# Optimization experiments

Hardware: AMD Instinct MI355X
Metric: run time of the kernel (lower is better)

## Reference

```python
import jax, jax.numpy as jnp
import numpy as np
import math

NUM_HEADS = 16


def setup_inputs() -> dict:
    key = jax.random.key(0)
    ks = jax.random.split(key, 7)
    B, S, D = 2, 2048, 1024
    scale = 1.0 / math.sqrt(D)
    return {
        "query": jax.random.normal(ks[0], (B, S, D), jnp.float32),
        "key": jax.random.normal(ks[1], (B, S, D), jnp.float32),
        "value": jax.random.normal(ks[2], (B, S, D), jnp.float32),
        "Wq": jax.random.normal(ks[3], (D, D), jnp.float32) * scale,
        "Wk": jax.random.normal(ks[4], (D, D), jnp.float32) * scale,
        "Wv": jax.random.normal(ks[5], (D, D), jnp.float32) * scale,
        "Wo": jax.random.normal(ks[6], (D, D), jnp.float32) * scale,
    }


def reference(query, key, value, Wq, Wk, Wv, Wo):
    B, Sq, D = query.shape
    Sk = key.shape[1]
    H = NUM_HEADS
    dk = D // H
    # torch Linear (no bias): y = x @ W.T
    q = (query @ Wq.T).reshape(B, Sq, H, dk).transpose(0, 2, 1, 3)  # [B,H,Sq,dk]
    k = (key @ Wk.T).reshape(B, Sk, H, dk).transpose(0, 2, 1, 3)
    v = (value @ Wv.T).reshape(B, Sk, H, dk).transpose(0, 2, 1, 3)
    scores = jnp.einsum("bhqd,bhkd->bhqk", q, k) / jnp.sqrt(jnp.float32(dk))
    causal = jnp.tril(jnp.ones((Sq, Sk), dtype=bool))  # mask_future=True
    scores = jnp.where(causal[None, None], scores, jnp.float32(-1e9))
    p = jax.nn.softmax(scores, axis=-1)
    x = jnp.einsum("bhqk,bhkd->bhqd", p, v)  # [B,H,Sq,dk]
    x = x.transpose(0, 2, 1, 3).reshape(B, Sq, D)
    return x @ Wo.T
```

## Files before the change

kernel.cpp:

```cpp
#include <hip/hip_runtime.h>
#include <hip/hip_bf16.h>
#include <stdint.h>

#define D_MODEL 1024
#define NHEADS  16
#define DK      64
#define SEQ     2048
#define BATCH   2

typedef __bf16 bf16x8 __attribute__((ext_vector_type(8)));
typedef __bf16 bf16x4 __attribute__((ext_vector_type(4)));
typedef float  f32x4  __attribute__((ext_vector_type(4)));

__device__ __forceinline__ void async_copy16(const void* g, void* l) {
  __builtin_amdgcn_global_load_lds(
      (__attribute__((address_space(1))) void*)g,
      (__attribute__((address_space(3))) void*)l, 16, 0, 0);
}

__global__ void cast_all(const float* __restrict__ q, const float* __restrict__ k,
                         const float* __restrict__ v, const float* __restrict__ wq,
                         const float* __restrict__ wk, const float* __restrict__ wv,
                         const float* __restrict__ wo,
                         __bf16* __restrict__ oq, __bf16* __restrict__ ok,
                         __bf16* __restrict__ ov, __bf16* __restrict__ owq,
                         __bf16* __restrict__ owk, __bf16* __restrict__ owv,
                         __bf16* __restrict__ owo) {
  constexpr unsigned Q4 = (unsigned)(BATCH * SEQ * D_MODEL) / 4;
  constexpr unsigned W4 = (unsigned)(D_MODEL * D_MODEL) / 4;
  unsigned i = blockIdx.x * 256u + threadIdx.x;
  const float* in; __bf16* out; unsigned off;
  if (i < 3 * Q4) {
    unsigned z = i >> 20; off = i & (Q4 - 1);
    in  = z == 0 ? q : z == 1 ? k : v;
    out = z == 0 ? oq : z == 1 ? ok : ov;
  } else {
    unsigned j = i - 3 * Q4;
    unsigned z = j >> 18; off = j & (W4 - 1);
    in  = z == 0 ? wq : z == 1 ? wk : z == 2 ? wv : wo;
    out = z == 0 ? owq : z == 1 ? owk : z == 2 ? owv : owo;
  }
  float4 val = *(const float4*)(in + (size_t)off * 4);
  bf16x4 o;
  o.x = (__bf16)val.x; o.y = (__bf16)val.y; o.z = (__bf16)val.z; o.w = (__bf16)val.w;
  *(bf16x4*)(out + (size_t)off * 4) = o;
}

__global__ __launch_bounds__(256, 3)
void gemm_proj(const __bf16* __restrict__ A0, const __bf16* __restrict__ A1, const __bf16* __restrict__ A2,
               const __bf16* __restrict__ B0, const __bf16* __restrict__ B1, const __bf16* __restrict__ B2,
               __bf16* __restrict__ Qp, __bf16* __restrict__ Kp, __bf16* __restrict__ Vt) {
  constexpr int K = D_MODEL, N = D_MODEL;
  const int zi = blockIdx.z;
  const __bf16* A; const __bf16* Bm;
  if (zi == 0)      { A = A0; Bm = B0; }
  else if (zi == 1) { A = A1; Bm = B1; }
  else              { A = A2; Bm = B2; }

  __shared__ __align__(16) char smem[34816];
  __bf16* Ash = (__bf16*)smem;
  __bf16* Bsh = (__bf16*)(smem + 16384);
  __bf16* Tr  = (__bf16*)smem;

  const int tid  = threadIdx.x;
  const int lane = tid & 63;
  const int w    = tid >> 6;
  const int quad = lane >> 4;
  const int l16  = lane & 15;
  const int wr   = w >> 1, wc = w & 1;
  const size_t m0 = (size_t)blockIdx.x * 128;
  const size_t n0 = (size_t)blockIdx.y * 128;

  f32x4 acc[4][4] = {};

  for (int k0 = 0; k0 < K; k0 += 64) {
#pragma unroll
    for (int it = 0; it < 4; ++it) {
      int slot = tid + it * 256;
      int row = slot >> 3, ch = slot & 7;
      async_copy16(A + (m0 + row) * K + k0 + ((ch ^ (row & 7)) * 8), &Ash[slot * 8]);
    }
#pragma unroll
    for (int it = 0; it < 4; ++it) {
      int slot = tid + it * 256;
      int row = slot >> 3, ch = slot & 7;
      async_copy16(Bm + (n0 + row) * K + k0 + ((ch ^ (row & 7)) * 8), &Bsh[slot * 8]);
    }
    __syncthreads();
#pragma unroll
    for (int kk = 0; kk < 2; ++kk) {
      bf16x8 af[4], bfr[4];
#pragma unroll
      for (int i = 0; i < 4; ++i) {
        int row = wr * 64 + i * 16 + l16;
        af[i] = *(const bf16x8*)&Ash[row * 64 + (((kk * 4 + quad) ^ (row & 7)) * 8)];
      }
#pragma unroll
      for (int j = 0; j < 4; ++j) {
        int row = wc * 64 + j * 16 + l16;
        bfr[j] = *(const bf16x8*)&Bsh[row * 64 + (((kk * 4 + quad) ^ (row & 7)) * 8)];
      }
#pragma unroll
      for (int i = 0; i < 4; ++i)
#pragma unroll
        for (int j = 0; j < 4; ++j)
          acc[i][j] = __builtin_amdgcn_mfma_f32_16x16x32_bf16(af[i], bfr[j], acc[i][j], 0, 0, 0);
    }
    __syncthreads();
  }

  if (zi != 2) {
    __bf16* C = (zi == 0) ? Qp : Kp;
#pragma unroll
    for (int i = 0; i < 4; ++i)
#pragma unroll
      for (int j = 0; j < 4; ++j)
#pragma unroll
        for (int r = 0; r < 4; ++r) {
          size_t row = m0 + wr * 64 + i * 16 + quad * 4 + r;
          size_t col = n0 + wc * 64 + j * 16 + l16;
          C[row * N + col] = (__bf16)acc[i][j][r];
        }
  } else {
#pragma unroll
    for (int i = 0; i < 4; ++i)
#pragma unroll
      for (int j = 0; j < 4; ++j)
#pragma unroll
        for (int r = 0; r < 4; ++r)
          Tr[(wc * 64 + j * 16 + l16) * 136 + (wr * 64 + i * 16 + quad * 4 + r)] =
              (__bf16)acc[i][j][r];
    __syncthreads();
    const int b_  = (int)(m0 >> 11);
    const int sl0 = (int)(m0 & 2047);
#pragma unroll
    for (int it = 0; it < 8; ++it) {
      int slot = tid + it * 256;
      int d = slot >> 4, sc = slot & 15;
      *(int4*)&Vt[((size_t)(b_ * D_MODEL) + n0 + d) * SEQ + sl0 + sc * 8] =
          *(const int4*)&Tr[d * 136 + sc * 8];
    }
  }
}

__global__ __launch_bounds__(256, 2)
void gemm_out(const __bf16* __restrict__ A, const __bf16* __restrict__ Bm,
              float* __restrict__ C) {
  constexpr int BM = 64, BN = 128, K = D_MODEL, N = D_MODEL;
  __shared__ __bf16 Ash[BM * 64];
  __shared__ __bf16 Bsh[BN * 64];

  const int tid  = threadIdx.x;
  const int lane = tid & 63;
  const int w    = tid >> 6;
  const int quad = lane >> 4;
  const int l16  = lane & 15;
  const int wr   = w >> 1, wc = w & 1;
  const size_t m0 = (size_t)blockIdx.x * BM;
  const size_t n0 = (size_t)blockIdx.y * BN;

  f32x4 acc[2][4] = {};

  for (int k0 = 0; k0 < K; k0 += 64) {
#pragma unroll
    for (int it = 0; it < 2; ++it) {
      int slot = tid + it * 256;
      int row = slot >> 3, ch = slot & 7;
      async_copy16(A + (m0 + row) * K + k0 + ((ch ^ (row & 7)) * 8), &Ash[slot * 8]);
    }
#pragma unroll
    for (int it = 0; it < 4; ++it) {
      int slot = tid + it * 256;
      int row = slot >> 3, ch = slot & 7;
      async_copy16(Bm + (n0 + row) * K + k0 + ((ch ^ (row & 7)) * 8), &Bsh[slot * 8]);
    }
    __syncthreads();
#pragma unroll
    for (int kk = 0; kk < 2; ++kk) {
      bf16x8 af[2], bfr[4];
#pragma unroll
      for (int i = 0; i < 2; ++i) {
        int row = wr * 32 + i * 16 + l16;
        af[i] = *(const bf16x8*)&Ash[row * 64 + (((kk * 4 + quad) ^ (row & 7)) * 8)];
      }
#pragma unroll
      for (int j = 0; j < 4; ++j) {
        int row = wc * 64 + j * 16 + l16;
        bfr[j] = *(const bf16x8*)&Bsh[row * 64 + (((kk * 4 + quad) ^ (row & 7)) * 8)];
      }
#pragma unroll
      for (int i = 0; i < 2; ++i)
#pragma unroll
        for (int j = 0; j < 4; ++j)
          acc[i][j] = __builtin_amdgcn_mfma_f32_16x16x32_bf16(af[i], bfr[j], acc[i][j], 0, 0, 0);
    }
    __syncthreads();
  }

#pragma unroll
  for (int i = 0; i < 2; ++i)
#pragma unroll
    for (int j = 0; j < 4; ++j)
#pragma unroll
      for (int r = 0; r < 4; ++r) {
        size_t row = m0 + wr * 32 + i * 16 + quad * 4 + r;
        size_t col = n0 + wc * 64 + j * 16 + l16;
        C[row * N + col] = acc[i][j][r];
      }
}

#define PS_W 40

__global__ __launch_bounds__(256, 3)
void attn_kernel(const __bf16* __restrict__ Qp, const __bf16* __restrict__ Kp,
                 const __bf16* __restrict__ Vt, __bf16* __restrict__ Xo) {
  __shared__ __bf16 Kb[2 * 2 * 64 * 32];
  __shared__ __bf16 Vb[2 * 2 * 64 * 32];
  __shared__ __bf16 Ps[4 * 32 * PS_W];
  __shared__ float  Xch[2 * 16 * 66];
  __shared__ float  Lsum[2 * 32];

  const int tid  = threadIdx.x;
  const int lane = tid & 63;
  const int w    = tid >> 6;
  const int qh   = w >> 1, kh = w & 1;
  const int quad = lane >> 4;
  const int l16  = lane & 15;
  const int bh   = blockIdx.x;
  const int qt   = 31 - blockIdx.y;
  const int b    = bh >> 4, h = bh & 15;
  const int q0   = qt * 64;
  const size_t baseRow = (size_t)b * SEQ;
  const int colBase = h * DK;

  const int srow = w * 16 + (lane >> 2);
  const int sk   = (lane & 3) * 8;
  const int skz  = (((lane & 3) ^ ((lane >> 3) & 3)) * 8);
  const int swz  = (l16 >> 1) & 3;

  const float c1 = 0.18033688011f;
  const float c2 = -23.083120654f;

  bf16x8 aq[2][2];
  {
    const __bf16* qrow = Qp + (baseRow + q0 + qh * 32 + l16) * D_MODEL + colBase;
#pragma unroll
    for (int mt = 0; mt < 2; ++mt)
#pragma unroll
      for (int kd = 0; kd < 2; ++kd)
        aq[mt][kd] = *(const bf16x8*)(qrow + (size_t)mt * 16 * D_MODEL + kd * 32 + quad * 8);
  }

  f32x4 oacc[2][4] = {};
  float plsum[2][4] = {};

  {
    const __bf16* kbase = Kp + (baseRow + srow) * D_MODEL + colBase + skz;
    async_copy16(kbase,      &Kb[0 * 2048 + srow * 32 + sk]);
    async_copy16(kbase + 32, &Kb[1 * 2048 + srow * 32 + sk]);
    const __bf16* vbase = Vt + ((size_t)b * D_MODEL + colBase + srow) * SEQ + skz;
    async_copy16(vbase,      &Vb[0 * 2048 + srow * 32 + sk]);
    async_copy16(vbase + 32, &Vb[1 * 2048 + srow * 32 + sk]);
  }

  for (int j = 0; j <= qt; ++j) {
    const int bf = j & 1;
    __syncthreads();

    if (j < qt) {
      const int nb = bf ^ 1;
      const __bf16* kbase = Kp + (baseRow + (size_t)(j + 1) * 64 + srow) * D_MODEL + colBase + skz;
      async_copy16(kbase,      &Kb[(nb * 2 + 0) * 2048 + srow * 32 + sk]);
      async_copy16(kbase + 32, &Kb[(nb * 2 + 1) * 2048 + srow * 32 + sk]);
      const __bf16* vbase = Vt + ((size_t)b * D_MODEL + colBase + srow) * SEQ + (size_t)(j + 1) * 64 + skz;
      async_copy16(vbase,      &Vb[(nb * 2 + 0) * 2048 + srow * 32 + sk]);
      async_copy16(vbase + 32, &Vb[(nb * 2 + 1) * 2048 + srow * 32 + sk]);
    }

    f32x4 sacc[2][2] = {};
    __builtin_amdgcn_s_setprio(1);
#pragma unroll
    for (int kd = 0; kd < 2; ++kd) {
      bf16x8 bk0 = *(const bf16x8*)&Kb[(bf * 2 + kd) * 2048 + (kh * 32 + l16) * 32 + (quad ^ swz) * 8];
      bf16x8 bk1 = *(const bf16x8*)&Kb[(bf * 2 + kd) * 2048 + (kh * 32 + 16 + l16) * 32 + (quad ^ swz) * 8];
      sacc[0][0] = __builtin_amdgcn_mfma_f32_16x16x32_bf16(aq[0][kd], bk0, sacc[0][0], 0, 0, 0);
      sacc[0][1] = __builtin_amdgcn_mfma_f32_16x16x32_bf16(aq[0][kd], bk1, sacc[0][1], 0, 0, 0);
      sacc[1][0] = __builtin_amdgcn_mfma_f32_16x16x32_bf16(aq[1][kd], bk0, sacc[1][0], 0, 0, 0);
      sacc[1][1] = __builtin_amdgcn_mfma_f32_16x16x32_bf16(aq[1][kd], bk1, sacc[1][1], 0, 0, 0);
    }
    __builtin_amdgcn_s_setprio(0);

    const bool diag = (j == qt);
#pragma unroll
    for (int mt = 0; mt < 2; ++mt)
#pragma unroll
      for (int nt2 = 0; nt2 < 2; ++nt2)
#pragma unroll
        for (int r = 0; r < 4; ++r) {
          float arg = fmaf(sacc[mt][nt2][r], c1, c2);
          if (diag) {
            int rowg = q0 + qh * 32 + mt * 16 + quad * 4 + r;
            int colg = j * 64 + kh * 32 + nt2 * 16 + l16;
            if (colg > rowg) arg = -1e30f;
          }
          float p = __builtin_amdgcn_exp2f(arg);
          plsum[mt][r] += p;
          Ps[(w * 32 + mt * 16 + quad * 4 + r) * PS_W + nt2 * 16 + l16] = (__bf16)p;
        }

    bf16x8 bv[4];
    __builtin_amdgcn_s_setprio(1);
#pragma unroll
    for (int nt = 0; nt < 4; ++nt)
      bv[nt] = *(const bf16x8*)&Vb[(bf * 2 + kh) * 2048 + (nt * 16 + l16) * 32 + (quad ^ swz) * 8];
#pragma unroll
    for (int mt = 0; mt < 2; ++mt) {
      bf16x8 ap = *(const bf16x8*)&Ps[(w * 32 + mt * 16 + l16) * PS_W + quad * 8];
#pragma unroll
      for (int nt = 0; nt < 4; ++nt)
        oacc[mt][nt] = __builtin_amdgcn_mfma_f32_16x16x32_bf16(ap, bv[nt], oacc[mt][nt], 0, 0, 0);
    }
    __builtin_amdgcn_s_setprio(0);
  }

  float lred[2][4];
#pragma unroll
  for (int mt = 0; mt < 2; ++mt)
#pragma unroll
    for (int r = 0; r < 4; ++r) {
      float l = plsum[mt][r];
      for (int off = 1; off < 16; off <<= 1) l += __shfl_xor(l, off, 64);
      lred[mt][r] = l;
    }

#pragma unroll
  for (int mt = 0; mt < 2; ++mt) {
    __syncthreads();
    if (kh == 1) {
#pragma unroll
      for (int nt = 0; nt < 4; ++nt)
#pragma unroll
        for (int r = 0; r < 4; ++r)
          Xch[(qh * 16 + quad * 4 + r) * 66 + nt * 16 + l16] = oacc[mt][nt][r];
#pragma unroll
      for (int r = 0; r < 4; ++r)
        Lsum[qh * 32 + mt * 16 + quad * 4 + r] = lred[mt][r];
    }
    __syncthreads();
    if (kh == 0) {
#pragma unroll
      for (int r = 0; r < 4; ++r) {
        float lt  = lred[mt][r] + Lsum[qh * 32 + mt * 16 + quad * 4 + r];
        float inv = 1.0f / lt;
        size_t row = baseRow + q0 + qh * 32 + mt * 16 + quad * 4 + r;
#pragma unroll
        for (int nt = 0; nt < 4; ++nt) {
          float o = oacc[mt][nt][r] + Xch[(qh * 16 + quad * 4 + r) * 66 + nt * 16 + l16];
          Xo[row * D_MODEL + colBase + nt * 16 + l16] = (__bf16)(o * inv);
        }
      }
    }
  }
}

extern "C" void kernel_launch(void* const* d_in, const int* in_sizes, int n_in,
                              void* d_out, int out_size, void* d_ws, size_t ws_size,
                              hipStream_t stream) {
  const float* q  = (const float*)d_in[0];
  const float* k  = (const float*)d_in[1];
  const float* v  = (const float*)d_in[2];
  const float* wq = (const float*)d_in[3];
  const float* wk = (const float*)d_in[4];
  const float* wv = (const float*)d_in[5];
  const float* wo = (const float*)d_in[6];
  float* out = (float*)d_out;

  const size_t MD = (size_t)BATCH * SEQ * D_MODEL;
  const size_t WD = (size_t)D_MODEL * D_MODEL;
  __bf16* ws  = (__bf16*)d_ws;
  __bf16* Qp  = ws;
  __bf16* Kp  = Qp + MD;
  __bf16* Vt  = Kp + MD;
  __bf16* Xa  = Vt + MD;
  __bf16* qbf = Xa + MD;
  __bf16* kbf = qbf + MD;
  __bf16* vbf = kbf + MD;
  __bf16* wqb = vbf + MD;
  __bf16* wkb = wqb + WD;
  __bf16* wvb = wkb + WD;
  __bf16* wob = wvb + WD;

  cast_all<<<16384, 256, 0, stream>>>(q, k, v, wq, wk, wv, wo,
                                      qbf, kbf, vbf, wqb, wkb, wvb, wob);

  gemm_proj<<<dim3(32, 8, 3), 256, 0, stream>>>(
      qbf, kbf, vbf, wqb, wkb, wvb, Qp, Kp, Vt);

  attn_kernel<<<dim3(BATCH * NHEADS, 32), 256, 0, stream>>>(Qp, Kp, Vt, Xa);

  gemm_out<<<dim3(64, 8), 256, 0, stream>>>(Xa, wob, out);
}
```

Baseline: 193.1 us.

## Enlarge attention query tile to 128 rows with 8-wave blocks

The attention kernel now processes 128 query rows per block using 512 threads (8 waves) instead of 64 rows with 256 threads, and the grid is halved along the query dimension. The K and V tile copies are now split across all threads, so each staged K/V tile serves twice as many queries, which cuts global traffic. Shared memory is merged into one aliased buffer so the epilogue scratch reuses the K buffer and occupancy stays acceptable. The risks are coarser causal load balancing with fewer, larger blocks, and two diagonal tiles per block that need masking.

```diff
diff --git a/kernel.cpp b/kernel.cpp
--- a/kernel.cpp
+++ b/kernel.cpp
@@ -211,14 +211,15 @@
 
 #define PS_W 40
 
-__global__ __launch_bounds__(256, 3)
+__global__ __launch_bounds__(512, 4)
 void attn_kernel(const __bf16* __restrict__ Qp, const __bf16* __restrict__ Kp,
                  const __bf16* __restrict__ Vt, __bf16* __restrict__ Xo) {
-  __shared__ __bf16 Kb[2 * 2 * 64 * 32];
-  __shared__ __bf16 Vb[2 * 2 * 64 * 32];
-  __shared__ __bf16 Ps[4 * 32 * PS_W];
-  __shared__ float  Xch[2 * 16 * 66];
-  __shared__ float  Lsum[2 * 32];
+  __shared__ __align__(16) char smem[53248];
+  __bf16* Kb  = (__bf16*)smem;
+  __bf16* Vb  = (__bf16*)(smem + 16384);
+  __bf16* Ps  = (__bf16*)(smem + 32768);
+  float*  Xch  = (float*)smem;
+  float*  Lsum = (float*)(smem + 16896);
 
   const int tid  = threadIdx.x;
   const int lane = tid & 63;
@@ -227,15 +228,16 @@
   const int quad = lane >> 4;
   const int l16  = lane & 15;
   const int bh   = blockIdx.x;
-  const int qt   = 31 - blockIdx.y;
+  const int qt   = 15 - blockIdx.y;
   const int b    = bh >> 4, h = bh & 15;
-  const int q0   = qt * 64;
+  const int q0   = qt * 128;
   const size_t baseRow = (size_t)b * SEQ;
   const int colBase = h * DK;
 
-  const int srow = w * 16 + (lane >> 2);
-  const int sk   = (lane & 3) * 8;
-  const int skz  = (((lane & 3) ^ ((lane >> 3) & 3)) * 8);
+  const int skd  = tid >> 8;
+  const int srow = (tid >> 2) & 63;
+  const int sk   = (tid & 3) * 8;
+  const int skz  = (((tid & 3) ^ ((tid >> 3) & 3)) * 8);
   const int swz  = (l16 >> 1) & 3;
 
   const float c1 = 0.18033688011f;
@@ -254,27 +256,25 @@
   f32x4 oacc[2][4] = {};
   float plsum[2][4] = {};
 
+  const int jmax = 2 * qt + 1;
+
   {
-    const __bf16* kbase = Kp + (baseRow + srow) * D_MODEL + colBase + skz;
-    async_copy16(kbase,      &Kb[0 * 2048 + srow * 32 + sk]);
-    async_copy16(kbase + 32, &Kb[1 * 2048 + srow * 32 + sk]);
-    const __bf16* vbase = Vt + ((size_t)b * D_MODEL + colBase + srow) * SEQ + skz;
-    async_copy16(vbase,      &Vb[0 * 2048 + srow * 32 + sk]);
-    async_copy16(vbase + 32, &Vb[1 * 2048 + srow * 32 + sk]);
-  }
-
-  for (int j = 0; j <= qt; ++j) {
+    async_copy16(Kp + (baseRow + srow) * D_MODEL + colBase + skd * 32 + skz,
+                 &Kb[skd * 2048 + srow * 32 + sk]);
+    async_copy16(Vt + ((size_t)b * D_MODEL + colBase + srow) * SEQ + skd * 32 + skz,
+                 &Vb[skd * 2048 + srow * 32 + sk]);
+  }
+
+  for (int j = 0; j <= jmax; ++j) {
     const int bf = j & 1;
     __syncthreads();
 
-    if (j < qt) {
+    if (j < jmax) {
       const int nb = bf ^ 1;
-      const __bf16* kbase = Kp + (baseRow + (size_t)(j + 1) * 64 + srow) * D_MODEL + colBase + skz;
-      async_copy16(kbase,      &Kb[(nb * 2 + 0) * 2048 + srow * 32 + sk]);
-      async_copy16(kbase + 32, &Kb[(nb * 2 + 1) * 2048 + srow * 32 + sk]);
-      const __bf16* vbase = Vt + ((size_t)b * D_MODEL + colBase + srow) * SEQ + (size_t)(j + 1) * 64 + skz;
-      async_copy16(vbase,      &Vb[(nb * 2 + 0) * 2048 + srow * 32 + sk]);
-      async_copy16(vbase + 32, &Vb[(nb * 2 + 1) * 2048 + srow * 32 + sk]);
+      async_copy16(Kp + (baseRow + (size_t)(j + 1) * 64 + srow) * D_MODEL + colBase + skd * 32 + skz,
+                   &Kb[(nb * 2 + skd) * 2048 + srow * 32 + sk]);
+      async_copy16(Vt + ((size_t)b * D_MODEL + colBase + srow) * SEQ + (size_t)(j + 1) * 64 + skd * 32 + skz,
+                   &Vb[(nb * 2 + skd) * 2048 + srow * 32 + sk]);
     }
 
     f32x4 sacc[2][2] = {};
@@ -290,7 +290,7 @@
     }
     __builtin_amdgcn_s_setprio(0);
 
-    const bool diag = (j == qt);
+    const bool diag = (j >= 2 * qt);
 #pragma unroll
     for (int mt = 0; mt < 2; ++mt)
 #pragma unroll
@@ -396,7 +396,7 @@
   gemm_proj<<<dim3(32, 8, 3), 256, 0, stream>>>(
       qbf, kbf, vbf, wqb, wkb, wvb, Qp, Kp, Vt);
 
-  attn_kernel<<<dim3(BATCH * NHEADS, 32), 256, 0, stream>>>(Qp, Kp, Vt, Xa);
+  attn_kernel<<<dim3(BATCH * NHEADS, 16), 512, 0, stream>>>(Qp, Kp, Vt, Xa);
 
   gemm_out<<<dim3(64, 8), 256, 0, stream>>>(Xa, wob, out);
 }
```

After: 201.1 us. 4.2% more time.

## Compute transposed scores to keep P in registers, dropping LDS staging

Applied to the files above, without the earlier changes.

The QK^T MFMA operands are swapped so each lane holds score values along the key dimension. The bf16 probabilities can then be packed straight into the A operand of the PV MFMA, with no round trip through a shared-memory P buffer. V fragments are rebuilt from two swizzled 4-element LDS reads to match the new k ordering. The row-sum reduction shrinks to two shuffles. The epilogue aliases shared memory, cutting LDS to 32KB, and launch bounds rise to 4 blocks per CU. The risk is more register pressure under the tighter occupancy bound, plus subtle index bugs in the transposed masking and layout.

```diff
diff --git a/kernel.cpp b/kernel.cpp
--- a/kernel.cpp
+++ b/kernel.cpp
@@ -209,16 +209,14 @@
       }
 }
 
-#define PS_W 40
-
-__global__ __launch_bounds__(256, 3)
+__global__ __launch_bounds__(256, 4)
 void attn_kernel(const __bf16* __restrict__ Qp, const __bf16* __restrict__ Kp,
                  const __bf16* __restrict__ Vt, __bf16* __restrict__ Xo) {
-  __shared__ __bf16 Kb[2 * 2 * 64 * 32];
-  __shared__ __bf16 Vb[2 * 2 * 64 * 32];
-  __shared__ __bf16 Ps[4 * 32 * PS_W];
-  __shared__ float  Xch[2 * 16 * 66];
-  __shared__ float  Lsum[2 * 32];
+  __shared__ __align__(16) char smem[32768];
+  __bf16* Kb = (__bf16*)smem;
+  __bf16* Vb = (__bf16*)(smem + 16384);
+  float*  Xch = (float*)smem;
+  float*  Ls  = (float*)(smem + 8448);
 
   const int tid  = threadIdx.x;
   const int lane = tid & 63;
@@ -252,7 +250,10 @@
   }
 
   f32x4 oacc[2][4] = {};
-  float plsum[2][4] = {};
+  float plsum[2] = {};
+
+  const int e1 = (((quad >> 1) ^ swz) * 8) + (quad & 1) * 4;
+  const int e2 = ((((quad >> 1) + 2) ^ swz) * 8) + (quad & 1) * 4;
 
   {
     const __bf16* kbase = Kp + (baseRow + srow) * D_MODEL + colBase + skz;
@@ -283,55 +284,55 @@
     for (int kd = 0; kd < 2; ++kd) {
       bf16x8 bk0 = *(const bf16x8*)&Kb[(bf * 2 + kd) * 2048 + (kh * 32 + l16) * 32 + (quad ^ swz) * 8];
       bf16x8 bk1 = *(const bf16x8*)&Kb[(bf * 2 + kd) * 2048 + (kh * 32 + 16 + l16) * 32 + (quad ^ swz) * 8];
-      sacc[0][0] = __builtin_amdgcn_mfma_f32_16x16x32_bf16(aq[0][kd], bk0, sacc[0][0], 0, 0, 0);
-      sacc[0][1] = __builtin_amdgcn_mfma_f32_16x16x32_bf16(aq[0][kd], bk1, sacc[0][1], 0, 0, 0);
-      sacc[1][0] = __builtin_amdgcn_mfma_f32_16x16x32_bf16(aq[1][kd], bk0, sacc[1][0], 0, 0, 0);
-      sacc[1][1] = __builtin_amdgcn_mfma_f32_16x16x32_bf16(aq[1][kd], bk1, sacc[1][1], 0, 0, 0);
+      sacc[0][0] = __builtin_amdgcn_mfma_f32_16x16x32_bf16(bk0, aq[0][kd], sacc[0][0], 0, 0, 0);
+      sacc[0][1] = __builtin_amdgcn_mfma_f32_16x16x32_bf16(bk0, aq[1][kd], sacc[0][1], 0, 0, 0);
+      sacc[1][0] = __builtin_amdgcn_mfma_f32_16x16x32_bf16(bk1, aq[0][kd], sacc[1][0], 0, 0, 0);
+      sacc[1][1] = __builtin_amdgcn_mfma_f32_16x16x32_bf16(bk1, aq[1][kd], sacc[1][1], 0, 0, 0);
     }
     __builtin_amdgcn_s_setprio(0);
 
     const bool diag = (j == qt);
+    bf16x8 pa[2];
 #pragma unroll
     for (int mt = 0; mt < 2; ++mt)
 #pragma unroll
-      for (int nt2 = 0; nt2 < 2; ++nt2)
+      for (int st = 0; st < 2; ++st)
 #pragma unroll
         for (int r = 0; r < 4; ++r) {
-          float arg = fmaf(sacc[mt][nt2][r], c1, c2);
+          float arg = fmaf(sacc[st][mt][r], c1, c2);
           if (diag) {
-            int rowg = q0 + qh * 32 + mt * 16 + quad * 4 + r;
-            int colg = j * 64 + kh * 32 + nt2 * 16 + l16;
+            int rowg = q0 + qh * 32 + mt * 16 + l16;
+            int colg = j * 64 + kh * 32 + st * 16 + quad * 4 + r;
             if (colg > rowg) arg = -1e30f;
           }
           float p = __builtin_amdgcn_exp2f(arg);
-          plsum[mt][r] += p;
-          Ps[(w * 32 + mt * 16 + quad * 4 + r) * PS_W + nt2 * 16 + l16] = (__bf16)p;
+          plsum[mt] += p;
+          pa[mt][st * 4 + r] = (__bf16)p;
         }
 
-    bf16x8 bv[4];
     __builtin_amdgcn_s_setprio(1);
 #pragma unroll
-    for (int nt = 0; nt < 4; ++nt)
-      bv[nt] = *(const bf16x8*)&Vb[(bf * 2 + kh) * 2048 + (nt * 16 + l16) * 32 + (quad ^ swz) * 8];
-#pragma unroll
-    for (int mt = 0; mt < 2; ++mt) {
-      bf16x8 ap = *(const bf16x8*)&Ps[(w * 32 + mt * 16 + l16) * PS_W + quad * 8];
-#pragma unroll
-      for (int nt = 0; nt < 4; ++nt)
-        oacc[mt][nt] = __builtin_amdgcn_mfma_f32_16x16x32_bf16(ap, bv[nt], oacc[mt][nt], 0, 0, 0);
+    for (int nt = 0; nt < 4; ++nt) {
+      const int rowb = (bf * 2 + kh) * 2048 + (nt * 16 + l16) * 32;
+      bf16x4 lo = *(const bf16x4*)&Vb[rowb + e1];
+      bf16x4 hi = *(const bf16x4*)&Vb[rowb + e2];
+      bf16x8 bv;
+      bv[0] = lo[0]; bv[1] = lo[1]; bv[2] = lo[2]; bv[3] = lo[3];
+      bv[4] = hi[0]; bv[5] = hi[1]; bv[6] = hi[2]; bv[7] = hi[3];
+      oacc[0][nt] = __builtin_amdgcn_mfma_f32_16x16x32_bf16(pa[0], bv, oacc[0][nt], 0, 0, 0);
+      oacc[1][nt] = __builtin_amdgcn_mfma_f32_16x16x32_bf16(pa[1], bv, oacc[1][nt], 0, 0, 0);
     }
     __builtin_amdgcn_s_setprio(0);
   }
 
-  float lred[2][4];
-#pragma unroll
-  for (int mt = 0; mt < 2; ++mt)
-#pragma unroll
-    for (int r = 0; r < 4; ++r) {
-      float l = plsum[mt][r];
-      for (int off = 1; off < 16; off <<= 1) l += __shfl_xor(l, off, 64);
-      lred[mt][r] = l;
-    }
+  float lred[2];
+#pragma unroll
+  for (int mt = 0; mt < 2; ++mt) {
+    float l = plsum[mt];
+    l += __shfl_xor(l, 16, 64);
+    l += __shfl_xor(l, 32, 64);
+    lred[mt] = l;
+  }
 
 #pragma unroll
   for (int mt = 0; mt < 2; ++mt) {
@@ -342,15 +343,13 @@
 #pragma unroll
         for (int r = 0; r < 4; ++r)
           Xch[(qh * 16 + quad * 4 + r) * 66 + nt * 16 + l16] = oacc[mt][nt][r];
-#pragma unroll
-      for (int r = 0; r < 4; ++r)
-        Lsum[qh * 32 + mt * 16 + quad * 4 + r] = lred[mt][r];
-    }
+    }
+    if (quad == 0) Ls[kh * 32 + qh * 16 + l16] = lred[mt];
     __syncthreads();
     if (kh == 0) {
 #pragma unroll
       for (int r = 0; r < 4; ++r) {
-        float lt  = lred[mt][r] + Lsum[qh * 32 + mt * 16 + quad * 4 + r];
+        float lt  = Ls[0 * 32 + qh * 16 + quad * 4 + r] + Ls[1 * 32 + qh * 16 + quad * 4 + r];
         float inv = 1.0f / lt;
         size_t row = baseRow + q0 + qh * 32 + mt * 16 + quad * 4 + r;
 #pragma unroll
```

Result: faster. 182.6 us, median of 2 (-5.4%).
